# Performance work log

Measured on AMD Instinct MI355X. Metric: run time of the kernel, lower is better.

The kernel has to match this reference:

```python
import jax, jax.numpy as jnp
import numpy as np

B, Q, K, H, DV = 16, 256, 256, 256, 256


def setup_inputs() -> dict:
    key = jax.random.key(0)
    ks = jax.random.split(key, 6)
    return {
        "queries": jax.random.normal(ks[0], (B, Q, H), dtype=jnp.float32),
        "keys": jax.random.normal(ks[1], (B, K, H), dtype=jnp.float32),
        "values": jax.random.normal(ks[2], (B, K, DV), dtype=jnp.float32),
        "W_q": jax.random.normal(ks[3], (H, H), dtype=jnp.float32) / np.sqrt(H),
        "W_k": jax.random.normal(ks[4], (H, H), dtype=jnp.float32) / np.sqrt(H),
        "w_v": jax.random.normal(ks[5], (H,), dtype=jnp.float32) / np.sqrt(H),
    }


def reference(queries, keys, values, W_q, W_k, w_v):
    # Linear projections (nn.Linear: x @ W.T), bias-free
    q = jnp.einsum("bqd,hd->bqh", queries, W_q)  # [B,Q,H]
    k = jnp.einsum("bkd,hd->bkh", keys, W_k)      # [B,K,H]
    # Broadcast add -> tanh -> scalar projection
    features = jnp.tanh(q[:, :, None, :] + k[:, None, :, :])  # [B,Q,K,H]
    scores = jnp.einsum("bqkh,h->bqk", features, w_v)          # [B,Q,K]
    attn = jax.nn.softmax(scores, axis=-1)                      # [B,Q,K]
    return jnp.einsum("bqk,bkv->bqv", attn, values)            # [B,Q,DV]
```

## Files before the change

### kernel.cpp

```cpp
#include <hip/hip_runtime.h>

#define Bn 16
#define Qn 256
#define Kn 256
#define Hn 256
#define DVn 256

constexpr float C2    = 2.8853900817779268f;
constexpr float LOG2E = 1.4426950408889634f;

__device__ __forceinline__ float fast_exp2(float x) { return __builtin_amdgcn_exp2f(x); }
__device__ __forceinline__ float fast_rcp(float x)  { return __builtin_amdgcn_rcpf(x); }

__global__ __launch_bounds__(256)
void proj_exp_kernel(const float* __restrict__ q, const float* __restrict__ kx,
                     const float* __restrict__ wq, const float* __restrict__ wk,
                     float* __restrict__ Eq, float* __restrict__ Ek)
{
    const int z = blockIdx.z;
    const float* A = z ? kx : q;
    const float* W = z ? wk : wq;
    const int m0 = blockIdx.y * 64;
    const int n0 = blockIdx.x * 64;
    __shared__ __align__(16) float As[2][16][68];
    __shared__ __align__(16) float Bs[2][16][68];
    const int tid = threadIdx.x;
    const int tx = tid & 15, ty = tid >> 4;
    const int lr = tid >> 2, lk4 = (tid & 3) * 4;
    const float* Arow = A + (size_t)(m0 + lr) * Hn + lk4;
    const float* Wrow = W + (size_t)(n0 + lr) * Hn + lk4;
    {
        float4 a = *(const float4*)(Arow);
        float4 w = *(const float4*)(Wrow);
        As[0][lk4+0][lr] = a.x; As[0][lk4+1][lr] = a.y; As[0][lk4+2][lr] = a.z; As[0][lk4+3][lr] = a.w;
        Bs[0][lk4+0][lr] = w.x; Bs[0][lk4+1][lr] = w.y; Bs[0][lk4+2][lr] = w.z; Bs[0][lk4+3][lr] = w.w;
    }
    __syncthreads();
    float acc[4][4] = {};
    int cur = 0;
    for (int k0 = 0; k0 < Hn; k0 += 16) {
        float4 an, wn;
        const bool more = (k0 + 16 < Hn);
        if (more) {
            an = *(const float4*)(Arow + k0 + 16);
            wn = *(const float4*)(Wrow + k0 + 16);
        }
        #pragma unroll
        for (int kk = 0; kk < 16; ++kk) {
            float4 av = *(const float4*)&As[cur][kk][ty*4];
            float4 bv = *(const float4*)&Bs[cur][kk][tx*4];
            const float ar[4] = {av.x, av.y, av.z, av.w};
            const float br[4] = {bv.x, bv.y, bv.z, bv.w};
            #pragma unroll
            for (int i = 0; i < 4; ++i)
                #pragma unroll
                for (int j = 0; j < 4; ++j)
                    acc[i][j] = fmaf(ar[i], br[j], acc[i][j]);
        }
        if (more) {
            const int nxt = cur ^ 1;
            As[nxt][lk4+0][lr] = an.x; As[nxt][lk4+1][lr] = an.y; As[nxt][lk4+2][lr] = an.z; As[nxt][lk4+3][lr] = an.w;
            Bs[nxt][lk4+0][lr] = wn.x; Bs[nxt][lk4+1][lr] = wn.y; Bs[nxt][lk4+2][lr] = wn.z; Bs[nxt][lk4+3][lr] = wn.w;
            __syncthreads();
            cur = nxt;
        }
    }
    #pragma unroll
    for (int i = 0; i < 4; ++i) {
        float4 o;
        o.x = fast_exp2(C2 * acc[i][0]);
        o.y = fast_exp2(C2 * acc[i][1]);
        o.z = fast_exp2(C2 * acc[i][2]);
        o.w = fast_exp2(C2 * acc[i][3]);
        if (z == 0) {
            *(float4*)(Eq + (size_t)(m0 + ty*4 + i) * Hn + n0 + tx*4) = o;
        } else {
            const int m  = m0 + ty*4 + i;
            const int bq = m >> 8, kk2 = m & 255;
            const int h  = n0 + tx*4;
            *(float4*)(Ek + (size_t)bq * (Kn*Hn) + (size_t)(h >> 2) * (Kn*4) + kk2*4) = o;
        }
    }
}

__global__ __launch_bounds__(256)
void fused_attn_kernel(const float* __restrict__ Eq, const float* __restrict__ Ek,
                       const float* __restrict__ wv, const float* __restrict__ V,
                       float* __restrict__ out)
{
    const int b  = blockIdx.y;
    const int q0 = blockIdx.x * 4;
    __shared__ __align__(16) float sEq[4 * 256];
    __shared__ __align__(16) float swv[256];
    __shared__ __align__(16) float sP[4 * 260];
    __shared__ float sredM[4][4];
    __shared__ float sredS[4][4];
    const int tid = threadIdx.x;
    {
        const int q = tid >> 6, h4 = (tid & 63) * 4;
        float4 v = *(const float4*)(Eq + (size_t)(b*Qn + q0 + q) * Hn + h4);
        *(float4*)&sEq[q*256 + h4] = v;
        swv[tid] = wv[tid];
    }
    __syncthreads();

    float sc[4] = {0.f, 0.f, 0.f, 0.f};
    const float* ekp = Ek + (size_t)b * (Kn*Hn) + (size_t)tid * 4;
    for (int hg = 0; hg < 64; hg += 2) {
        const float4 e0 = *(const float4*)(ekp + hg * (Kn*4));
        const float4 e1 = *(const float4*)(ekp + hg * (Kn*4) + (Kn*4));
        const int h0 = hg * 4;
        const float4 wa = *(const float4*)&swv[h0];
        const float4 wb = *(const float4*)&swv[h0 + 4];
        #pragma unroll
        for (int q = 0; q < 4; ++q) {
            const float4 ea = *(const float4*)&sEq[q*256 + h0];
            const float4 eb = *(const float4*)&sEq[q*256 + h0 + 4];
            float a = sc[q];
            a = fmaf(wa.x, fast_rcp(fmaf(ea.x, e0.x, 1.f)), a);
            a = fmaf(wa.y, fast_rcp(fmaf(ea.y, e0.y, 1.f)), a);
            a = fmaf(wa.z, fast_rcp(fmaf(ea.z, e0.z, 1.f)), a);
            a = fmaf(wa.w, fast_rcp(fmaf(ea.w, e0.w, 1.f)), a);
            a = fmaf(wb.x, fast_rcp(fmaf(eb.x, e1.x, 1.f)), a);
            a = fmaf(wb.y, fast_rcp(fmaf(eb.y, e1.y, 1.f)), a);
            a = fmaf(wb.z, fast_rcp(fmaf(eb.z, e1.z, 1.f)), a);
            a = fmaf(wb.w, fast_rcp(fmaf(eb.w, e1.w, 1.f)), a);
            sc[q] = a;
        }
    }

    const int w = tid >> 6, lane = tid & 63;
    #pragma unroll
    for (int q = 0; q < 4; ++q) {
        sc[q] = -2.0f * sc[q];
        float mx = sc[q];
        #pragma unroll
        for (int off = 32; off; off >>= 1) mx = fmaxf(mx, __shfl_xor(mx, off, 64));
        if (lane == 0) sredM[q][w] = mx;
    }
    __syncthreads();
    float p[4];
    #pragma unroll
    for (int q = 0; q < 4; ++q) {
        const float mx = fmaxf(fmaxf(sredM[q][0], sredM[q][1]),
                               fmaxf(sredM[q][2], sredM[q][3]));
        p[q] = fast_exp2(LOG2E * (sc[q] - mx));
        float s = p[q];
        #pragma unroll
        for (int off = 32; off; off >>= 1) s += __shfl_xor(s, off, 64);
        if (lane == 0) sredS[q][w] = s;
        sP[q*260 + tid] = p[q];
    }
    __syncthreads();
    float rinv[4];
    #pragma unroll
    for (int q = 0; q < 4; ++q)
        rinv[q] = fast_rcp(sredS[q][0] + sredS[q][1] + sredS[q][2] + sredS[q][3]);

    float acc[4] = {0.f, 0.f, 0.f, 0.f};
    const float* Vb = V + (size_t)b * Kn * DVn + tid;
    for (int k = 0; k < Kn; k += 4) {
        float vv[4];
        #pragma unroll
        for (int j = 0; j < 4; ++j) vv[j] = Vb[(size_t)(k + j) * DVn];
        #pragma unroll
        for (int q = 0; q < 4; ++q) {
            const float4 pq = *(const float4*)&sP[q*260 + k];
            float a = acc[q];
            a = fmaf(pq.x, vv[0], a);
            a = fmaf(pq.y, vv[1], a);
            a = fmaf(pq.z, vv[2], a);
            a = fmaf(pq.w, vv[3], a);
            acc[q] = a;
        }
    }
    float* ob = out + (size_t)(b*Qn + q0) * DVn + tid;
    #pragma unroll
    for (int q = 0; q < 4; ++q)
        ob[(size_t)q * DVn] = acc[q] * rinv[q];
}

extern "C" void kernel_launch(void* const* d_in, const int* in_sizes, int n_in,
                              void* d_out, int out_size, void* d_ws, size_t ws_size,
                              hipStream_t stream) {
    const float* queries = (const float*)d_in[0];
    const float* keys    = (const float*)d_in[1];
    const float* values  = (const float*)d_in[2];
    const float* W_q     = (const float*)d_in[3];
    const float* W_k     = (const float*)d_in[4];
    const float* w_v     = (const float*)d_in[5];
    float* out = (float*)d_out;

    float* Eq = (float*)d_ws;
    float* Ek = Eq + (size_t)Bn * Qn * Hn;

    proj_exp_kernel<<<dim3(4, 64, 2), 256, 0, stream>>>(queries, keys, W_q, W_k, Eq, Ek);
    fused_attn_kernel<<<dim3(64, 16), 256, 0, stream>>>(Eq, Ek, w_v, values, out);
}
```

Measured before the change: 133.6 us.

## Store Ek as bf16, repack V, and process 8 queries per block

Ek is written in bf16, halving its traffic in the attention kernel. V is repacked into k4-interleaved float4s by an extra z-slice of the projection launch, so the PV loop issues vector loads with prefetch. Each attention block now handles 8 queries instead of 4, doubling reuse of every Ek and V load, and the Ek loads are software-prefetched. The trade-offs are bf16 rounding error on exp(2k) inside the tanh, more registers, and half as many blocks (512).

```diff
diff --git a/kernel.cpp b/kernel.cpp
--- a/kernel.cpp
+++ b/kernel.cpp
@@ -12,19 +12,42 @@
 __device__ __forceinline__ float fast_exp2(float x) { return __builtin_amdgcn_exp2f(x); }
 __device__ __forceinline__ float fast_rcp(float x)  { return __builtin_amdgcn_rcpf(x); }
 
+__device__ __forceinline__ unsigned short f2bf(float x) {
+    unsigned u = __float_as_uint(x);
+    u += 0x7fffu + ((u >> 16) & 1u);
+    return (unsigned short)(u >> 16);
+}
+
 __global__ __launch_bounds__(256)
 void proj_exp_kernel(const float* __restrict__ q, const float* __restrict__ kx,
                      const float* __restrict__ wq, const float* __restrict__ wk,
-                     float* __restrict__ Eq, float* __restrict__ Ek)
+                     const float* __restrict__ V,
+                     float* __restrict__ Eq, unsigned short* __restrict__ Ekb,
+                     float* __restrict__ Vp)
 {
     const int z = blockIdx.z;
+    const int tid = threadIdx.x;
+    if (z == 2) {
+        const int L = blockIdx.y * 4 + blockIdx.x;
+        #pragma unroll
+        for (int j = 0; j < 4; ++j) {
+            const int p   = L * 1024 + j * 256 + tid;
+            const int bk4 = p >> 8;
+            const int dv  = p & 255;
+            const int b   = bk4 >> 6, k4 = bk4 & 63;
+            const float* src = V + ((size_t)(b * Kn + 4 * k4)) * DVn + dv;
+            float4 o;
+            o.x = src[0 * DVn]; o.y = src[1 * DVn]; o.z = src[2 * DVn]; o.w = src[3 * DVn];
+            *(float4*)(Vp + (size_t)p * 4) = o;
+        }
+        return;
+    }
     const float* A = z ? kx : q;
     const float* W = z ? wk : wq;
     const int m0 = blockIdx.y * 64;
     const int n0 = blockIdx.x * 64;
     __shared__ __align__(16) float As[2][16][68];
     __shared__ __align__(16) float Bs[2][16][68];
-    const int tid = threadIdx.x;
     const int tx = tid & 15, ty = tid >> 4;
     const int lr = tid >> 2, lk4 = (tid & 3) * 4;
     const float* Arow = A + (size_t)(m0 + lr) * Hn + lk4;
@@ -77,107 +100,123 @@
         } else {
             const int m  = m0 + ty*4 + i;
             const int bq = m >> 8, kk2 = m & 255;
-            const int h  = n0 + tx*4;
-            *(float4*)(Ek + (size_t)bq * (Kn*Hn) + (size_t)(h >> 2) * (Kn*4) + kk2*4) = o;
+            const int hg = (n0 + tx*4) >> 2;
+            ushort4 s;
+            s.x = f2bf(o.x); s.y = f2bf(o.y); s.z = f2bf(o.z); s.w = f2bf(o.w);
+            *(ushort4*)(Ekb + ((size_t)(bq * 64 + hg) * 256 + kk2) * 4) = s;
         }
     }
 }
 
 __global__ __launch_bounds__(256)
-void fused_attn_kernel(const float* __restrict__ Eq, const float* __restrict__ Ek,
-                       const float* __restrict__ wv, const float* __restrict__ V,
+void fused_attn_kernel(const float* __restrict__ Eq, const unsigned short* __restrict__ Ekb,
+                       const float* __restrict__ wv, const float* __restrict__ Vp,
                        float* __restrict__ out)
 {
     const int b  = blockIdx.y;
-    const int q0 = blockIdx.x * 4;
-    __shared__ __align__(16) float sEq[4 * 256];
+    const int q0 = blockIdx.x * 8;
+    __shared__ __align__(16) float sEq[8 * 256];
     __shared__ __align__(16) float swv[256];
-    __shared__ __align__(16) float sP[4 * 260];
-    __shared__ float sredM[4][4];
-    __shared__ float sredS[4][4];
+    __shared__ __align__(16) float sP[8 * 260];
+    __shared__ float sredM[8][4];
+    __shared__ float sredS[8][4];
     const int tid = threadIdx.x;
-    {
-        const int q = tid >> 6, h4 = (tid & 63) * 4;
-        float4 v = *(const float4*)(Eq + (size_t)(b*Qn + q0 + q) * Hn + h4);
-        *(float4*)&sEq[q*256 + h4] = v;
-        swv[tid] = wv[tid];
-    }
-    __syncthreads();
-
-    float sc[4] = {0.f, 0.f, 0.f, 0.f};
-    const float* ekp = Ek + (size_t)b * (Kn*Hn) + (size_t)tid * 4;
-    for (int hg = 0; hg < 64; hg += 2) {
-        const float4 e0 = *(const float4*)(ekp + hg * (Kn*4));
-        const float4 e1 = *(const float4*)(ekp + hg * (Kn*4) + (Kn*4));
-        const int h0 = hg * 4;
-        const float4 wa = *(const float4*)&swv[h0];
-        const float4 wb = *(const float4*)&swv[h0 + 4];
-        #pragma unroll
-        for (int q = 0; q < 4; ++q) {
-            const float4 ea = *(const float4*)&sEq[q*256 + h0];
-            const float4 eb = *(const float4*)&sEq[q*256 + h0 + 4];
-            float a = sc[q];
-            a = fmaf(wa.x, fast_rcp(fmaf(ea.x, e0.x, 1.f)), a);
-            a = fmaf(wa.y, fast_rcp(fmaf(ea.y, e0.y, 1.f)), a);
-            a = fmaf(wa.z, fast_rcp(fmaf(ea.z, e0.z, 1.f)), a);
-            a = fmaf(wa.w, fast_rcp(fmaf(ea.w, e0.w, 1.f)), a);
-            a = fmaf(wb.x, fast_rcp(fmaf(eb.x, e1.x, 1.f)), a);
-            a = fmaf(wb.y, fast_rcp(fmaf(eb.y, e1.y, 1.f)), a);
-            a = fmaf(wb.z, fast_rcp(fmaf(eb.z, e1.z, 1.f)), a);
-            a = fmaf(wb.w, fast_rcp(fmaf(eb.w, e1.w, 1.f)), a);
-            sc[q] = a;
-        }
+    #pragma unroll
+    for (int r = 0; r < 2; ++r) {
+        const int i = tid + r * 256;
+        const int qq = i >> 6, h4 = (i & 63) * 4;
+        *(float4*)&sEq[qq*256 + h4] = *(const float4*)(Eq + (size_t)(b*Qn + q0 + qq) * Hn + h4);
+    }
+    swv[tid] = wv[tid];
+    __syncthreads();
+
+    float sc[8] = {};
+    const uint2* ekp = (const uint2*)Ekb + (size_t)b * 16384 + tid;
+    uint2 e[4];
+    #pragma unroll
+    for (int g = 0; g < 4; ++g) e[g] = ekp[g * 256];
+    for (int it = 0; it < 16; ++it) {
+        uint2 en[4];
+        if (it < 15) {
+            #pragma unroll
+            for (int g = 0; g < 4; ++g) en[g] = ekp[(4*(it+1) + g) * 256];
+        }
+        const int h0 = it * 16;
+        float ek[16];
+        #pragma unroll
+        for (int g = 0; g < 4; ++g) {
+            ek[4*g+0] = __uint_as_float(e[g].x << 16);
+            ek[4*g+1] = __uint_as_float(e[g].x & 0xFFFF0000u);
+            ek[4*g+2] = __uint_as_float(e[g].y << 16);
+            ek[4*g+3] = __uint_as_float(e[g].y & 0xFFFF0000u);
+        }
+        #pragma unroll
+        for (int qq = 0; qq < 8; ++qq) {
+            float a = sc[qq];
+            #pragma unroll
+            for (int g = 0; g < 4; ++g) {
+                const float4 ea = *(const float4*)&sEq[qq*256 + h0 + 4*g];
+                const float4 wa = *(const float4*)&swv[h0 + 4*g];
+                a = fmaf(wa.x, fast_rcp(fmaf(ea.x, ek[4*g+0], 1.f)), a);
+                a = fmaf(wa.y, fast_rcp(fmaf(ea.y, ek[4*g+1], 1.f)), a);
+                a = fmaf(wa.z, fast_rcp(fmaf(ea.z, ek[4*g+2], 1.f)), a);
+                a = fmaf(wa.w, fast_rcp(fmaf(ea.w, ek[4*g+3], 1.f)), a);
+            }
+            sc[qq] = a;
+        }
+        #pragma unroll
+        for (int g = 0; g < 4; ++g) e[g] = en[g];
     }
 
     const int w = tid >> 6, lane = tid & 63;
     #pragma unroll
-    for (int q = 0; q < 4; ++q) {
-        sc[q] = -2.0f * sc[q];
-        float mx = sc[q];
+    for (int qq = 0; qq < 8; ++qq) {
+        sc[qq] = -2.0f * sc[qq];
+        float mx = sc[qq];
         #pragma unroll
         for (int off = 32; off; off >>= 1) mx = fmaxf(mx, __shfl_xor(mx, off, 64));
-        if (lane == 0) sredM[q][w] = mx;
-    }
-    __syncthreads();
-    float p[4];
-    #pragma unroll
-    for (int q = 0; q < 4; ++q) {
-        const float mx = fmaxf(fmaxf(sredM[q][0], sredM[q][1]),
-                               fmaxf(sredM[q][2], sredM[q][3]));
-        p[q] = fast_exp2(LOG2E * (sc[q] - mx));
-        float s = p[q];
+        if (lane == 0) sredM[qq][w] = mx;
+    }
+    __syncthreads();
+    #pragma unroll
+    for (int qq = 0; qq < 8; ++qq) {
+        const float mx = fmaxf(fmaxf(sredM[qq][0], sredM[qq][1]),
+                               fmaxf(sredM[qq][2], sredM[qq][3]));
+        const float p = fast_exp2(LOG2E * (sc[qq] - mx));
+        float s = p;
         #pragma unroll
         for (int off = 32; off; off >>= 1) s += __shfl_xor(s, off, 64);
-        if (lane == 0) sredS[q][w] = s;
-        sP[q*260 + tid] = p[q];
-    }
-    __syncthreads();
-    float rinv[4];
-    #pragma unroll
-    for (int q = 0; q < 4; ++q)
-        rinv[q] = fast_rcp(sredS[q][0] + sredS[q][1] + sredS[q][2] + sredS[q][3]);
-
-    float acc[4] = {0.f, 0.f, 0.f, 0.f};
-    const float* Vb = V + (size_t)b * Kn * DVn + tid;
-    for (int k = 0; k < Kn; k += 4) {
-        float vv[4];
-        #pragma unroll
-        for (int j = 0; j < 4; ++j) vv[j] = Vb[(size_t)(k + j) * DVn];
-        #pragma unroll
-        for (int q = 0; q < 4; ++q) {
-            const float4 pq = *(const float4*)&sP[q*260 + k];
-            float a = acc[q];
-            a = fmaf(pq.x, vv[0], a);
-            a = fmaf(pq.y, vv[1], a);
-            a = fmaf(pq.z, vv[2], a);
-            a = fmaf(pq.w, vv[3], a);
-            acc[q] = a;
-        }
+        if (lane == 0) sredS[qq][w] = s;
+        sP[qq*260 + tid] = p;
+    }
+    __syncthreads();
+    float rinv[8];
+    #pragma unroll
+    for (int qq = 0; qq < 8; ++qq)
+        rinv[qq] = fast_rcp(sredS[qq][0] + sredS[qq][1] + sredS[qq][2] + sredS[qq][3]);
+
+    float acc[8] = {};
+    const float4* vp = (const float4*)Vp + (size_t)b * 64 * 256 + tid;
+    float4 vv = vp[0];
+    for (int k4 = 0; k4 < 64; ++k4) {
+        float4 vn;
+        if (k4 < 63) vn = vp[(k4 + 1) * 256];
+        #pragma unroll
+        for (int qq = 0; qq < 8; ++qq) {
+            const float4 pq = *(const float4*)&sP[qq*260 + 4*k4];
+            float a = acc[qq];
+            a = fmaf(pq.x, vv.x, a);
+            a = fmaf(pq.y, vv.y, a);
+            a = fmaf(pq.z, vv.z, a);
+            a = fmaf(pq.w, vv.w, a);
+            acc[qq] = a;
+        }
+        vv = vn;
     }
     float* ob = out + (size_t)(b*Qn + q0) * DVn + tid;
     #pragma unroll
-    for (int q = 0; q < 4; ++q)
-        ob[(size_t)q * DVn] = acc[q] * rinv[q];
+    for (int qq = 0; qq < 8; ++qq)
+        ob[(size_t)qq * DVn] = acc[qq] * rinv[qq];
 }
 
 extern "C" void kernel_launch(void* const* d_in, const int* in_sizes, int n_in,
@@ -191,9 +230,11 @@
     const float* w_v     = (const float*)d_in[5];
     float* out = (float*)d_out;
 
-    float* Eq = (float*)d_ws;
-    float* Ek = Eq + (size_t)Bn * Qn * Hn;
-
-    proj_exp_kernel<<<dim3(4, 64, 2), 256, 0, stream>>>(queries, keys, W_q, W_k, Eq, Ek);
-    fused_attn_kernel<<<dim3(64, 16), 256, 0, stream>>>(Eq, Ek, w_v, values, out);
-}
+    float*          Eq  = (float*)d_ws;
+    unsigned short* Ekb = (unsigned short*)(Eq + (size_t)Bn * Qn * Hn);
+    float*          Vp  = (float*)(Ekb + (size_t)Bn * Kn * Hn);
+
+    proj_exp_kernel<<<dim3(4, 64, 3), 256, 0, stream>>>(queries, keys, W_q, W_k, values,
+                                                        Eq, Ekb, Vp);
+    fused_attn_kernel<<<dim3(32, 16), 256, 0, stream>>>(Eq, Ekb, w_v, Vp, out);
+}
```

Measured after the change: 138.4 us. 1.04x slower.
